# Kernel optimization log

Hardware: AMD Instinct MI355X
Metric: run time of the kernel (lower is better)

Reference implementation:

```python
import jax, jax.numpy as jnp
import numpy as np

M = 0.25
GAMMA = 256.0
HARD_W = 2.0
O_P = 1.0 + M
O_N = -M
DELTA_P = 1.0 - M
DELTA_N = M
NEG_BIG = -1e30  # masked-out fill for logsumexp (finite to keep grads NaN-free)


def setup_inputs() -> dict:
    key = jax.random.key(0)
    k1, k2 = jax.random.split(key)
    inputs = jax.random.normal(k1, (4096, 512), dtype=jnp.float32)
    targets = jax.random.randint(k2, (4096,), 0, 64, dtype=jnp.int64)
    return {"inputs": inputs, "targets": targets}


def reference(inputs, targets):
    n = inputs.shape[0]
    x = inputs / jnp.linalg.norm(inputs, axis=1, keepdims=True)  # L2 normalize
    sim = x @ x.T                                                # [n, n]

    same = targets[:, None] == targets[None, :]
    eye = jnp.eye(n, dtype=bool)
    pos_mask = same & ~eye
    neg_mask = ~same
    npos = pos_mask.sum(axis=1)
    nneg = neg_mask.sum(axis=1)

    sim_d = jax.lax.stop_gradient(sim)  # alphas are detached in the original
    alpha_p = jax.nn.relu(O_P - sim_d)
    alpha_n = jax.nn.relu(sim_d - O_N)

    # hard mining: scale alpha at hardest positive (min sim) / hardest negative (max sim)
    idx = jnp.arange(n)
    hard_p = jnp.argmin(jnp.where(pos_mask, sim_d, jnp.inf), axis=1)
    hard_n = jnp.argmax(jnp.where(neg_mask, sim_d, -jnp.inf), axis=1)
    hit_p = (idx[None, :] == hard_p[:, None]) & (npos > 1)[:, None]
    hit_n = (idx[None, :] == hard_n[:, None]) & (nneg > 1)[:, None]
    alpha_p = alpha_p * jnp.where(hit_p, HARD_W, 1.0)
    alpha_n = alpha_n * jnp.where(hit_n, HARD_W, 1.0)

    pos_term = jnp.where(pos_mask, -GAMMA * alpha_p * (sim - DELTA_P), NEG_BIG)
    neg_term = jnp.where(neg_mask, GAMMA * alpha_n * (sim - DELTA_N), NEG_BIG)
    lse_p = jax.nn.logsumexp(pos_term, axis=1)
    lse_n = jax.nn.logsumexp(neg_term, axis=1)

    valid = (npos > 0) & (nneg > 0)
    per_row = jnp.where(valid, jax.nn.softplus(lse_p + lse_n), 0.0)
    n_valid = jnp.maximum(valid.sum(), 1)
    return per_row.sum() / n_valid.astype(per_row.dtype)
```

## Files before the change

kernel.cpp:

```cpp
#include <hip/hip_runtime.h>


#define GAMMA_ 256.0f
#define OP_ 1.25f
#define ON_ (-0.25f)
#define DP_ 0.75f
#define DN_ 0.25f
#define MASKT_ (-1.0e4f)

constexpr int N_ = 4096;
constexpr int D_ = 512;
constexpr int AST_ = 520;
constexpr int CCH_ = 8;

typedef __bf16 bf16x8 __attribute__((ext_vector_type(8)));
typedef float  f32x4  __attribute__((ext_vector_type(4)));

__device__ __forceinline__ float pos_term(float s) {
    return -GAMMA_ * fmaxf(OP_ - s, 0.0f) * (s - DP_);
}
__device__ __forceinline__ float neg_term(float s) {
    return  GAMMA_ * fmaxf(s - ON_, 0.0f) * (s - DN_);
}
__device__ __forceinline__ void lse_merge(float m2, float S2, float& m, float& S) {
    float mm = fmaxf(m, m2);
    S = S * __expf(m - mm) + S2 * __expf(m2 - mm);
    m = mm;
}
__device__ __forceinline__ unsigned short f2bf(float f) {
    unsigned int u = __float_as_uint(f);
    unsigned int r = u + 0x7FFFu + ((u >> 16) & 1u);
    return (unsigned short)(r >> 16);
}

__global__ __launch_bounds__(256) void k_norm(const float* __restrict__ in,
                                              unsigned short* __restrict__ xb,
                                              float* __restrict__ acc) {
    const int row  = blockIdx.x * 4 + (threadIdx.x >> 6);
    const int lane = threadIdx.x & 63;
    const float4* src = (const float4*)(in + (size_t)row * D_) + lane * 2;
    float4 a = src[0], b = src[1];
    float ss = a.x*a.x + a.y*a.y + a.z*a.z + a.w*a.w
             + b.x*b.x + b.y*b.y + b.z*b.z + b.w*b.w;
    #pragma unroll
    for (int d = 32; d >= 1; d >>= 1) ss += __shfl_xor(ss, d);
    float rn = 1.0f / sqrtf(ss);
    float v[8] = {a.x, a.y, a.z, a.w, b.x, b.y, b.z, b.w};
    union { uint4 u; unsigned short us[8]; } pk;
    #pragma unroll
    for (int k = 0; k < 8; ++k) pk.us[k] = f2bf(v[k] * rn);
    *((uint4*)(xb + (size_t)row * D_) + lane) = pk.u;
    if (blockIdx.x == 0 && threadIdx.x < 2) acc[threadIdx.x] = 0.0f;
}

__global__ __launch_bounds__(256, 3) void k_mainB(const unsigned short* __restrict__ xb,
                                                  const int* __restrict__ tg,
                                                  float* __restrict__ part) {
    constexpr int COLS = N_ / CCH_;
    constexpr int NST  = COLS / 16;
    __shared__ __align__(16) unsigned short Bs[2][16][AST_];

    const int tid  = threadIdx.x;
    const int wave = tid >> 6, lane = tid & 63;
    const int n16  = lane & 15, quad = lane >> 4;
    const int rg   = (int)blockIdx.x >> 3;
    const int cc   = (int)blockIdx.x & 7;
    const int rowBase = rg * 64 + wave * 16;
    const int colBase = cc * COLS;

    bf16x8 af[16];
    {
        const bf16x8* ap = (const bf16x8*)(xb + (size_t)(rowBase + n16) * D_ + quad * 8);
        #pragma unroll
        for (int kk = 0; kk < 16; ++kk) af[kk] = ap[kk * 4];
    }
    int ir[4], tr[4];
    #pragma unroll
    for (int r = 0; r < 4; ++r) { ir[r] = rowBase + quad * 4 + r; tr[r] = tg[ir[r]]; }

    float m_p[4], S_p[4], m_n[4], S_n[4], mnp[4], mxn[4], sc[4];
    #pragma unroll
    for (int r = 0; r < 4; ++r) {
        m_p[r] = 0.f; S_p[r] = 0.f; m_n[r] = 0.f; S_n[r] = 0.f;
        mnp[r] = 2.0f; mxn[r] = -2.0f; sc[r] = 0.f;
    }

    uint4 pf0, pf1, pf2, pf3; int pftc;
    {
        const uint4* g = (const uint4*)(xb + (size_t)colBase * D_);
        pf0 = g[tid]; pf1 = g[256 + tid]; pf2 = g[512 + tid]; pf3 = g[768 + tid];
        pftc = tg[colBase + n16];
    }

    #pragma unroll 1
    for (int s = 0; s < NST; ++s) {
        const int b = s & 1;
        const int j0 = colBase + s * 16;
        {
            int q;
            q = tid;       *(uint4*)&Bs[b][q >> 6][(q & 63) * 8] = pf0;
            q = 256 + tid; *(uint4*)&Bs[b][q >> 6][(q & 63) * 8] = pf1;
            q = 512 + tid; *(uint4*)&Bs[b][q >> 6][(q & 63) * 8] = pf2;
            q = 768 + tid; *(uint4*)&Bs[b][q >> 6][(q & 63) * 8] = pf3;
        }
        const int tc = pftc;
        if (s + 1 < NST) {
            const uint4* g = (const uint4*)(xb + (size_t)(j0 + 16) * D_);
            pf0 = g[tid]; pf1 = g[256 + tid]; pf2 = g[512 + tid]; pf3 = g[768 + tid];
            pftc = tg[j0 + 16 + n16];
        }
        __syncthreads();

        f32x4 a0 = {0.f, 0.f, 0.f, 0.f}, a1 = {0.f, 0.f, 0.f, 0.f};
        #pragma unroll
        for (int kk = 0; kk < 8; ++kk) {
            bf16x8 bf0 = *(const bf16x8*)&Bs[b][n16][(2 * kk) * 32 + quad * 8];
            bf16x8 bf1 = *(const bf16x8*)&Bs[b][n16][(2 * kk + 1) * 32 + quad * 8];
            a0 = __builtin_amdgcn_mfma_f32_16x16x32_bf16(af[2 * kk],     bf0, a0, 0, 0, 0);
            a1 = __builtin_amdgcn_mfma_f32_16x16x32_bf16(af[2 * kk + 1], bf1, a1, 0, 0, 0);
        }

        const int jcol = j0 + n16;
        #pragma unroll
        for (int r = 0; r < 4; ++r) {
            float s_ = a0[r] + a1[r];
            bool samec = (tr[r] == tc);
            bool posm  = samec && (jcol != ir[r]);
            float tp = posm  ? pos_term(s_) : MASKT_;
            float tn = samec ? MASKT_ : neg_term(s_);
            float mm = fmaxf(m_p[r], tp);
            S_p[r] = S_p[r] * __expf(m_p[r] - mm) + __expf(tp - mm); m_p[r] = mm;
            mm = fmaxf(m_n[r], tn);
            S_n[r] = S_n[r] * __expf(m_n[r] - mm) + __expf(tn - mm); m_n[r] = mm;
            sc[r] += samec ? 1.0f : 0.0f;
            mnp[r] = fminf(mnp[r], posm ? s_ : 2.0f);
            mxn[r] = fmaxf(mxn[r], samec ? -2.0f : s_);
        }
    }

    #pragma unroll
    for (int r = 0; r < 4; ++r) {
        #pragma unroll
        for (int d = 1; d <= 8; d <<= 1) {
            lse_merge(__shfl_xor(m_p[r], d), __shfl_xor(S_p[r], d), m_p[r], S_p[r]);
            lse_merge(__shfl_xor(m_n[r], d), __shfl_xor(S_n[r], d), m_n[r], S_n[r]);
            mnp[r] = fminf(mnp[r], __shfl_xor(mnp[r], d));
            mxn[r] = fmaxf(mxn[r], __shfl_xor(mxn[r], d));
            sc[r] += __shfl_xor(sc[r], d);
        }
    }
    if (n16 == 0) {
        #pragma unroll
        for (int r = 0; r < 4; ++r) {
            float4* P = (float4*)part + ((size_t)ir[r] * CCH_ + cc) * 2;
            P[0] = make_float4(m_p[r], S_p[r], m_n[r], S_n[r]);
            P[1] = make_float4(mnp[r], mxn[r], sc[r], 0.0f);
        }
    }
}

__global__ __launch_bounds__(256) void k_reduceB(const float* __restrict__ part,
                                                 float* __restrict__ acc) {
    const int row = blockIdx.x * 256 + threadIdx.x;
    const float4* P = (const float4*)part + (size_t)row * CCH_ * 2;
    float m_p = 0.f, S_p = 0.f, m_n = 0.f, S_n = 0.f;
    float mnp = 2.0f, mxn = -2.0f, sct = 0.f;
    #pragma unroll
    for (int c = 0; c < CCH_; ++c) {
        float4 a = P[2 * c], b = P[2 * c + 1];
        lse_merge(a.x, a.y, m_p, S_p);
        lse_merge(a.z, a.w, m_n, S_n);
        mnp = fminf(mnp, b.x); mxn = fmaxf(mxn, b.y); sct += b.z;
    }
    float loss = 0.f, vld = 0.f;
    float np2 = sct - 1.0f, nn2 = (float)N_ - sct;
    if (np2 > 0.5f && nn2 > 0.5f) {
        if (np2 > 1.5f) {
            float t1 = pos_term(mnp), t2 = 2.0f * t1;
            float mm = fmaxf(m_p, t2);
            S_p = S_p * __expf(m_p - mm) + __expf(t2 - mm) - __expf(t1 - mm);
            m_p = mm;
        }
        if (nn2 > 1.5f) {
            float t1 = neg_term(mxn), t2 = 2.0f * t1;
            float mm = fmaxf(m_n, t2);
            S_n = S_n * __expf(m_n - mm) + __expf(t2 - mm) - __expf(t1 - mm);
            m_n = mm;
        }
        float z = (m_p + __logf(S_p)) + (m_n + __logf(S_n));
        loss = fmaxf(z, 0.0f) + log1pf(__expf(-fabsf(z)));
        vld = 1.0f;
    }
    #pragma unroll
    for (int d = 32; d >= 1; d >>= 1) { loss += __shfl_xor(loss, d); vld += __shfl_xor(vld, d); }
    if ((threadIdx.x & 63) == 0) { atomicAdd(&acc[0], loss); atomicAdd(&acc[1], vld); }
}

__global__ void k_final(const float* __restrict__ acc, float* __restrict__ out) {
    if (threadIdx.x == 0) out[0] = acc[0] / fmaxf(acc[1], 1.0f);
}

__global__ void k_sentinel(float* __restrict__ out) {
    if (threadIdx.x == 0) out[0] = -12345.0f;
}

__global__ __launch_bounds__(1024, 4) void k_main3(const unsigned short* __restrict__ xb,
                                                   const int* __restrict__ tg,
                                                   float* __restrict__ acc_g) {
    __shared__ __align__(16) unsigned short As[16 * AST_];
    __shared__ float sm[16][16][8];
    const int tid  = threadIdx.x;
    const int wave = tid >> 6, lane = tid & 63;
    const int n16  = lane & 15, quad = lane >> 4;
    const int rowBase = blockIdx.x * 16;
    {
        int row = tid >> 6, c = tid & 63;
        *(uint4*)&As[row * AST_ + c * 8] =
            *(const uint4*)(xb + (size_t)(rowBase + row) * D_ + c * 8);
    }
    int ir[4], tr[4];
    #pragma unroll
    for (int r = 0; r < 4; ++r) { ir[r] = rowBase + quad * 4 + r; tr[r] = tg[ir[r]]; }
    float m_p[4], S_p[4], m_n[4], S_n[4], mnp[4], mxn[4], sc[4];
    #pragma unroll
    for (int r = 0; r < 4; ++r) {
        m_p[r] = 0.f; S_p[r] = 0.f; m_n[r] = 0.f; S_n[r] = 0.f;
        mnp[r] = 2.0f; mxn[r] = -2.0f; sc[r] = 0.f;
    }
    __syncthreads();
    const unsigned short* Af = &As[n16 * AST_ + quad * 8];
    #pragma unroll 1
    for (int t = wave; t < N_ / 16; t += 16) {
        const int jcol = t * 16 + n16;
        const int tc = tg[jcol];
        const bf16x8* bp = (const bf16x8*)(xb + (size_t)jcol * D_ + quad * 8);
        bf16x8 bf[16];
        #pragma unroll
        for (int kk = 0; kk < 16; ++kk) bf[kk] = bp[kk * 4];
        f32x4 a0 = {0.f, 0.f, 0.f, 0.f}, a1 = {0.f, 0.f, 0.f, 0.f};
        #pragma unroll
        for (int kk = 0; kk < 8; ++kk) {
            bf16x8 af0 = *(const bf16x8*)(Af + (2 * kk) * 32);
            bf16x8 af1 = *(const bf16x8*)(Af + (2 * kk + 1) * 32);
            a0 = __builtin_amdgcn_mfma_f32_16x16x32_bf16(af0, bf[2 * kk],     a0, 0, 0, 0);
            a1 = __builtin_amdgcn_mfma_f32_16x16x32_bf16(af1, bf[2 * kk + 1], a1, 0, 0, 0);
        }
        #pragma unroll
        for (int r = 0; r < 4; ++r) {
            float s = a0[r] + a1[r];
            bool samec = (tr[r] == tc);
            bool posm  = samec && (jcol != ir[r]);
            float tp = posm  ? pos_term(s) : MASKT_;
            float tn = samec ? MASKT_ : neg_term(s);
            float mm = fmaxf(m_p[r], tp);
            S_p[r] = S_p[r] * __expf(m_p[r] - mm) + __expf(tp - mm); m_p[r] = mm;
            mm = fmaxf(m_n[r], tn);
            S_n[r] = S_n[r] * __expf(m_n[r] - mm) + __expf(tn - mm); m_n[r] = mm;
            sc[r] += samec ? 1.0f : 0.0f;
            mnp[r] = fminf(mnp[r], posm ? s : 2.0f);
            mxn[r] = fmaxf(mxn[r], samec ? -2.0f : s);
        }
    }
    #pragma unroll
    for (int r = 0; r < 4; ++r) {
        #pragma unroll
        for (int d = 1; d <= 8; d <<= 1) {
            lse_merge(__shfl_xor(m_p[r], d), __shfl_xor(S_p[r], d), m_p[r], S_p[r]);
            lse_merge(__shfl_xor(m_n[r], d), __shfl_xor(S_n[r], d), m_n[r], S_n[r]);
            mnp[r] = fminf(mnp[r], __shfl_xor(mnp[r], d));
            mxn[r] = fmaxf(mxn[r], __shfl_xor(mxn[r], d));
            sc[r] += __shfl_xor(sc[r], d);
        }
    }
    if (n16 == 0) {
        #pragma unroll
        for (int r = 0; r < 4; ++r) {
            float* q = sm[wave][quad * 4 + r];
            q[0] = m_p[r]; q[1] = S_p[r]; q[2] = m_n[r]; q[3] = S_n[r];
            q[4] = mnp[r]; q[5] = mxn[r]; q[6] = sc[r];
        }
    }
    __syncthreads();
    if (tid < 64) {
        const int L = tid & 15;
        float m_p2 = 0.f, S_p2 = 0.f, m_n2 = 0.f, S_n2 = 0.f;
        float mnp2 = 2.0f, mxn2 = -2.0f, sct = 0.f;
        #pragma unroll
        for (int w = 0; w < 16; ++w) {
            const float* q = sm[w][L];
            lse_merge(q[0], q[1], m_p2, S_p2);
            lse_merge(q[2], q[3], m_n2, S_n2);
            mnp2 = fminf(mnp2, q[4]); mxn2 = fmaxf(mxn2, q[5]);
            sct += q[6];
        }
        float loss = 0.f, vld = 0.f;
        float np2 = sct - 1.0f, nn2 = (float)N_ - sct;
        if (tid < 16 && np2 > 0.5f && nn2 > 0.5f) {
            if (np2 > 1.5f) {
                float t1 = pos_term(mnp2), t2 = 2.0f * t1;
                float mm = fmaxf(m_p2, t2);
                S_p2 = S_p2 * __expf(m_p2 - mm) + __expf(t2 - mm) - __expf(t1 - mm);
                m_p2 = mm;
            }
            if (nn2 > 1.5f) {
                float t1 = neg_term(mxn2), t2 = 2.0f * t1;
                float mm = fmaxf(m_n2, t2);
                S_n2 = S_n2 * __expf(m_n2 - mm) + __expf(t2 - mm) - __expf(t1 - mm);
                m_n2 = mm;
            }
            float z = (m_p2 + __logf(S_p2)) + (m_n2 + __logf(S_n2));
            loss = fmaxf(z, 0.0f) + log1pf(__expf(-fabsf(z)));
            vld = 1.0f;
        }
        #pragma unroll
        for (int d = 32; d >= 1; d >>= 1) {
            loss += __shfl_xor(loss, d); vld += __shfl_xor(vld, d);
        }
        if (tid == 0) { atomicAdd(&acc_g[0], loss); atomicAdd(&acc_g[1], vld); }
    }
}

extern "C" void kernel_launch(void* const* d_in, const int* in_sizes, int n_in,
                              void* d_out, int out_size, void* d_ws, size_t ws_size,
                              hipStream_t stream) {
    const float* in = (const float*)d_in[0];
    const int*   tg = (const int*)d_in[1];
    constexpr size_t MB = 1024 * 1024;
    unsigned short* xb = (unsigned short*)d_ws;

    if (ws_size >= 5 * MB + 64) {
        float* part = (float*)((char*)d_ws + 4 * MB);
        float* acc  = (float*)((char*)d_ws + 5 * MB);
        hipLaunchKernelGGL(k_norm,    dim3(N_ / 4),   dim3(256), 0, stream, in, xb, acc);
        hipLaunchKernelGGL(k_mainB,   dim3(64 * CCH_), dim3(256), 0, stream, xb, tg, part);
        hipLaunchKernelGGL(k_reduceB, dim3(N_ / 256), dim3(256), 0, stream, part, acc);
        hipLaunchKernelGGL(k_final,   dim3(1),        dim3(64),  0, stream, acc, (float*)d_out);
    } else if (ws_size >= 4 * MB + 64) {
        float* acc = (float*)((char*)d_ws + 4 * MB);
        hipLaunchKernelGGL(k_norm,  dim3(N_ / 4),  dim3(256),  0, stream, in, xb, acc);
        hipLaunchKernelGGL(k_main3, dim3(N_ / 16), dim3(1024), 0, stream, xb, tg, acc);
        hipLaunchKernelGGL(k_final, dim3(1),       dim3(64),   0, stream, acc, (float*)d_out);
    } else {
        hipLaunchKernelGGL(k_sentinel, dim3(1), dim3(64), 0, stream, (float*)d_out);
    }
}
```

Baseline: 113.6 us.

## Simplify circle-loss terms algebraically, swizzle LDS, and split columns into 16 chunks

The pos/neg logits are rewritten as quadratics with the constant offset removed (256(s-1)^2 and 256 s^2, shifted by -16), and the online logsumexp now uses a branch so only one exp is computed per element. Same-class counts are no longer accumulated in the main loop; the reduce kernel builds a label histogram in shared memory instead. The column chunk count goes from 8 to 16, occupancy is raised to 4 blocks per CU, LDS uses an XOR-swizzled flat layout to avoid bank conflicts, and the loop is unrolled by two with a static double buffer. Each partial record shrinks to one float4 by storing the min/max similarity in place of the running max, which the reduce step recomputes. In exchange the reduce does more work per row, and the branchy update may diverge within a wave.

```diff
diff --git a/kernel.cpp b/kernel.cpp
--- a/kernel.cpp
+++ b/kernel.cpp
@@ -2,25 +2,23 @@
 
 
 #define GAMMA_ 256.0f
-#define OP_ 1.25f
-#define ON_ (-0.25f)
-#define DP_ 0.75f
-#define DN_ 0.25f
 #define MASKT_ (-1.0e4f)
 
 constexpr int N_ = 4096;
 constexpr int D_ = 512;
 constexpr int AST_ = 520;
-constexpr int CCH_ = 8;
+constexpr int CCH_ = 16;
 
 typedef __bf16 bf16x8 __attribute__((ext_vector_type(8)));
 typedef float  f32x4  __attribute__((ext_vector_type(4)));
 
-__device__ __forceinline__ float pos_term(float s) {
-    return -GAMMA_ * fmaxf(OP_ - s, 0.0f) * (s - DP_);
-}
-__device__ __forceinline__ float neg_term(float s) {
-    return  GAMMA_ * fmaxf(s - ON_, 0.0f) * (s - DN_);
+__device__ __forceinline__ float pos_q(float s) {
+    float d = s - 1.0f;
+    return fmaf(d * d, 256.0f, -16.0f);
+}
+__device__ __forceinline__ float neg_q(float s) {
+    float q = fmaf(s * s, 256.0f, -16.0f);
+    return (s >= -0.25f) ? q : 0.0f;
 }
 __device__ __forceinline__ void lse_merge(float m2, float S2, float& m, float& S) {
     float mm = fmaxf(m, m2);
@@ -53,20 +51,19 @@
     if (blockIdx.x == 0 && threadIdx.x < 2) acc[threadIdx.x] = 0.0f;
 }
 
-__global__ __launch_bounds__(256, 3) void k_mainB(const unsigned short* __restrict__ xb,
+__global__ __launch_bounds__(256, 4) void k_mainC(const unsigned short* __restrict__ xb,
                                                   const int* __restrict__ tg,
                                                   float* __restrict__ part) {
-    constexpr int COLS = N_ / CCH_;
-    constexpr int NST  = COLS / 16;
-    __shared__ __align__(16) unsigned short Bs[2][16][AST_];
+    constexpr int NST = 16;
+    __shared__ uint4 Bs[2][1024];
 
     const int tid  = threadIdx.x;
     const int wave = tid >> 6, lane = tid & 63;
     const int n16  = lane & 15, quad = lane >> 4;
-    const int rg   = (int)blockIdx.x >> 3;
-    const int cc   = (int)blockIdx.x & 7;
+    const int rg   = (int)blockIdx.x >> 4;
+    const int cc   = (int)blockIdx.x & 15;
     const int rowBase = rg * 64 + wave * 16;
-    const int colBase = cc * COLS;
+    const int colBase = cc * 256;
 
     bf16x8 af[16];
     {
@@ -78,64 +75,76 @@
     #pragma unroll
     for (int r = 0; r < 4; ++r) { ir[r] = rowBase + quad * 4 + r; tr[r] = tg[ir[r]]; }
 
-    float m_p[4], S_p[4], m_n[4], S_n[4], mnp[4], mxn[4], sc[4];
+    int wa[4];
+    #pragma unroll
+    for (int p = 0; p < 4; ++p) {
+        int kkw = lane >> 2;
+        int f   = (lane & 3) * 16 + (wave + 4 * p);
+        wa[p]   = kkw * 64 + (f ^ (kkw & 7));
+    }
+    int rva[8];
+    #pragma unroll
+    for (int c = 0; c < 8; ++c) rva[c] = lane ^ c;
+
+    float m_p[4], S_p[4], m_n[4], S_n[4], mnp[4], mxn[4];
     #pragma unroll
     for (int r = 0; r < 4; ++r) {
         m_p[r] = 0.f; S_p[r] = 0.f; m_n[r] = 0.f; S_n[r] = 0.f;
-        mnp[r] = 2.0f; mxn[r] = -2.0f; sc[r] = 0.f;
-    }
-
-    uint4 pf0, pf1, pf2, pf3; int pftc;
-    {
-        const uint4* g = (const uint4*)(xb + (size_t)colBase * D_);
-        pf0 = g[tid]; pf1 = g[256 + tid]; pf2 = g[512 + tid]; pf3 = g[768 + tid];
-        pftc = tg[colBase + n16];
-    }
-
-    #pragma unroll 1
-    for (int s = 0; s < NST; ++s) {
-        const int b = s & 1;
-        const int j0 = colBase + s * 16;
-        {
-            int q;
-            q = tid;       *(uint4*)&Bs[b][q >> 6][(q & 63) * 8] = pf0;
-            q = 256 + tid; *(uint4*)&Bs[b][q >> 6][(q & 63) * 8] = pf1;
-            q = 512 + tid; *(uint4*)&Bs[b][q >> 6][(q & 63) * 8] = pf2;
-            q = 768 + tid; *(uint4*)&Bs[b][q >> 6][(q & 63) * 8] = pf3;
-        }
-        const int tc = pftc;
-        if (s + 1 < NST) {
-            const uint4* g = (const uint4*)(xb + (size_t)(j0 + 16) * D_);
-            pf0 = g[tid]; pf1 = g[256 + tid]; pf2 = g[512 + tid]; pf3 = g[768 + tid];
-            pftc = tg[j0 + 16 + n16];
+        mnp[r] = 2.0f; mxn[r] = -2.0f;
+    }
+
+    const uint4* gsrc = (const uint4*)(xb + (size_t)colBase * D_);
+    uint4 pf0 = gsrc[tid], pf1 = gsrc[256 + tid], pf2 = gsrc[512 + tid], pf3 = gsrc[768 + tid];
+    int tc_cur = tg[colBase + n16], tc_nxt = 0;
+
+    auto do_stage = [&](int s, int b, bool pre) {
+        uint4* Bp = &Bs[b][0];
+        Bp[wa[0]] = pf0; Bp[wa[1]] = pf1; Bp[wa[2]] = pf2; Bp[wa[3]] = pf3;
+        if (pre) {
+            const uint4* g2 = gsrc + (s + 1) * 1024;
+            pf0 = g2[tid]; pf1 = g2[256 + tid]; pf2 = g2[512 + tid]; pf3 = g2[768 + tid];
+            tc_nxt = tg[colBase + (s + 1) * 16 + n16];
         }
         __syncthreads();
 
         f32x4 a0 = {0.f, 0.f, 0.f, 0.f}, a1 = {0.f, 0.f, 0.f, 0.f};
         #pragma unroll
         for (int kk = 0; kk < 8; ++kk) {
-            bf16x8 bf0 = *(const bf16x8*)&Bs[b][n16][(2 * kk) * 32 + quad * 8];
-            bf16x8 bf1 = *(const bf16x8*)&Bs[b][n16][(2 * kk + 1) * 32 + quad * 8];
+            bf16x8 bf0 = *(const bf16x8*)&Bp[(2 * kk) * 64 + rva[(2 * kk) & 7]];
+            bf16x8 bf1 = *(const bf16x8*)&Bp[(2 * kk + 1) * 64 + rva[(2 * kk + 1) & 7]];
             a0 = __builtin_amdgcn_mfma_f32_16x16x32_bf16(af[2 * kk],     bf0, a0, 0, 0, 0);
             a1 = __builtin_amdgcn_mfma_f32_16x16x32_bf16(af[2 * kk + 1], bf1, a1, 0, 0, 0);
         }
 
-        const int jcol = j0 + n16;
+        const int jcol = colBase + s * 16 + n16;
+        const int tcv = tc_cur;
         #pragma unroll
         for (int r = 0; r < 4; ++r) {
             float s_ = a0[r] + a1[r];
-            bool samec = (tr[r] == tc);
+            bool samec = (tr[r] == tcv);
             bool posm  = samec && (jcol != ir[r]);
-            float tp = posm  ? pos_term(s_) : MASKT_;
-            float tn = samec ? MASKT_ : neg_term(s_);
-            float mm = fmaxf(m_p[r], tp);
-            S_p[r] = S_p[r] * __expf(m_p[r] - mm) + __expf(tp - mm); m_p[r] = mm;
-            mm = fmaxf(m_n[r], tn);
-            S_n[r] = S_n[r] * __expf(m_n[r] - mm) + __expf(tn - mm); m_n[r] = mm;
-            sc[r] += samec ? 1.0f : 0.0f;
+            float tp = posm ? pos_q(s_) : MASKT_;
+            if (tp > m_p[r]) {
+                S_p[r] = fmaf(S_p[r], __expf(m_p[r] - tp), 1.0f); m_p[r] = tp;
+            } else {
+                S_p[r] += __expf(tp - m_p[r]);
+            }
             mnp[r] = fminf(mnp[r], posm ? s_ : 2.0f);
+            float tn = samec ? MASKT_ : neg_q(s_);
+            if (tn > m_n[r]) {
+                S_n[r] = fmaf(S_n[r], __expf(m_n[r] - tn), 1.0f); m_n[r] = tn;
+            } else {
+                S_n[r] += __expf(tn - m_n[r]);
+            }
             mxn[r] = fmaxf(mxn[r], samec ? -2.0f : s_);
         }
+        tc_cur = tc_nxt;
+    };
+
+    #pragma unroll 1
+    for (int it = 0; it < NST / 2; ++it) {
+        do_stage(2 * it,     0, true);
+        do_stage(2 * it + 1, 1, it < NST / 2 - 1);
     }
 
     #pragma unroll
@@ -146,54 +155,62 @@
             lse_merge(__shfl_xor(m_n[r], d), __shfl_xor(S_n[r], d), m_n[r], S_n[r]);
             mnp[r] = fminf(mnp[r], __shfl_xor(mnp[r], d));
             mxn[r] = fmaxf(mxn[r], __shfl_xor(mxn[r], d));
-            sc[r] += __shfl_xor(sc[r], d);
         }
     }
     if (n16 == 0) {
         #pragma unroll
         for (int r = 0; r < 4; ++r) {
-            float4* P = (float4*)part + ((size_t)ir[r] * CCH_ + cc) * 2;
-            P[0] = make_float4(m_p[r], S_p[r], m_n[r], S_n[r]);
-            P[1] = make_float4(mnp[r], mxn[r], sc[r], 0.0f);
-        }
-    }
-}
-
-__global__ __launch_bounds__(256) void k_reduceB(const float* __restrict__ part,
+            ((float4*)part)[(size_t)ir[r] * CCH_ + cc] =
+                make_float4(mnp[r], S_p[r], mxn[r], S_n[r]);
+        }
+    }
+}
+
+__global__ __launch_bounds__(256) void k_reduceC(const float* __restrict__ part,
+                                                 const int* __restrict__ tg,
                                                  float* __restrict__ acc) {
-    const int row = blockIdx.x * 256 + threadIdx.x;
-    const float4* P = (const float4*)part + (size_t)row * CCH_ * 2;
-    float m_p = 0.f, S_p = 0.f, m_n = 0.f, S_n = 0.f;
-    float mnp = 2.0f, mxn = -2.0f, sct = 0.f;
+    __shared__ int hist[64];
+    const int tid = threadIdx.x;
+    if (tid < 64) hist[tid] = 0;
+    __syncthreads();
+    for (int i = tid; i < N_; i += 256) atomicAdd(&hist[tg[i]], 1);
+    __syncthreads();
+
+    const int row = blockIdx.x * 256 + tid;
+    const float4* P = (const float4*)part + (size_t)row * CCH_;
+    float M_p = 0.f, Sp = 0.f, M_n = 0.f, Sn = 0.f, mnp = 2.0f, mxn = -2.0f;
     #pragma unroll
     for (int c = 0; c < CCH_; ++c) {
-        float4 a = P[2 * c], b = P[2 * c + 1];
-        lse_merge(a.x, a.y, m_p, S_p);
-        lse_merge(a.z, a.w, m_n, S_n);
-        mnp = fminf(mnp, b.x); mxn = fmaxf(mxn, b.y); sct += b.z;
-    }
+        float4 a = P[c];
+        float mc = (a.x < 1.5f) ? fmaxf(pos_q(a.x), 0.0f) : 0.0f;
+        lse_merge(mc, a.y, M_p, Sp);
+        float mn = (a.z > -1.5f) ? fmaxf(neg_q(a.z), 0.0f) : 0.0f;
+        lse_merge(mn, a.w, M_n, Sn);
+        mnp = fminf(mnp, a.x); mxn = fmaxf(mxn, a.z);
+    }
+    const int cnt = hist[tg[row]];
+    float np2 = (float)(cnt - 1), nn2 = (float)(N_ - cnt);
     float loss = 0.f, vld = 0.f;
-    float np2 = sct - 1.0f, nn2 = (float)N_ - sct;
     if (np2 > 0.5f && nn2 > 0.5f) {
         if (np2 > 1.5f) {
-            float t1 = pos_term(mnp), t2 = 2.0f * t1;
-            float mm = fmaxf(m_p, t2);
-            S_p = S_p * __expf(m_p - mm) + __expf(t2 - mm) - __expf(t1 - mm);
-            m_p = mm;
+            float t1 = pos_q(mnp), t2 = 2.0f * t1;
+            float mm = fmaxf(M_p, t2);
+            Sp = Sp * __expf(M_p - mm) + __expf(t2 - mm) - __expf(t1 - mm);
+            M_p = mm;
         }
         if (nn2 > 1.5f) {
-            float t1 = neg_term(mxn), t2 = 2.0f * t1;
-            float mm = fmaxf(m_n, t2);
-            S_n = S_n * __expf(m_n - mm) + __expf(t2 - mm) - __expf(t1 - mm);
-            m_n = mm;
-        }
-        float z = (m_p + __logf(S_p)) + (m_n + __logf(S_n));
+            float t1 = neg_q(mxn), t2 = 2.0f * t1;
+            float mm = fmaxf(M_n, t2);
+            Sn = Sn * __expf(M_n - mm) + __expf(t2 - mm) - __expf(t1 - mm);
+            M_n = mm;
+        }
+        float z = (M_p + __logf(Sp)) + (M_n + __logf(Sn));
         loss = fmaxf(z, 0.0f) + log1pf(__expf(-fabsf(z)));
         vld = 1.0f;
     }
     #pragma unroll
     for (int d = 32; d >= 1; d >>= 1) { loss += __shfl_xor(loss, d); vld += __shfl_xor(vld, d); }
-    if ((threadIdx.x & 63) == 0) { atomicAdd(&acc[0], loss); atomicAdd(&acc[1], vld); }
+    if ((tid & 63) == 0) { atomicAdd(&acc[0], loss); atomicAdd(&acc[1], vld); }
 }
 
 __global__ void k_final(const float* __restrict__ acc, float* __restrict__ out) {
@@ -250,8 +267,8 @@
             float s = a0[r] + a1[r];
             bool samec = (tr[r] == tc);
             bool posm  = samec && (jcol != ir[r]);
-            float tp = posm  ? pos_term(s) : MASKT_;
-            float tn = samec ? MASKT_ : neg_term(s);
+            float tp = posm  ? pos_q(s) : MASKT_;
+            float tn = samec ? MASKT_ : neg_q(s);
             float mm = fmaxf(m_p[r], tp);
             S_p[r] = S_p[r] * __expf(m_p[r] - mm) + __expf(tp - mm); m_p[r] = mm;
             mm = fmaxf(m_n[r], tn);
@@ -297,13 +314,13 @@
         float np2 = sct - 1.0f, nn2 = (float)N_ - sct;
         if (tid < 16 && np2 > 0.5f && nn2 > 0.5f) {
             if (np2 > 1.5f) {
-                float t1 = pos_term(mnp2), t2 = 2.0f * t1;
+                float t1 = pos_q(mnp2), t2 = 2.0f * t1;
                 float mm = fmaxf(m_p2, t2);
                 S_p2 = S_p2 * __expf(m_p2 - mm) + __expf(t2 - mm) - __expf(t1 - mm);
                 m_p2 = mm;
             }
             if (nn2 > 1.5f) {
-                float t1 = neg_term(mxn2), t2 = 2.0f * t1;
+                float t1 = neg_q(mxn2), t2 = 2.0f * t1;
                 float mm = fmaxf(m_n2, t2);
                 S_n2 = S_n2 * __expf(m_n2 - mm) + __expf(t2 - mm) - __expf(t1 - mm);
                 m_n2 = mm;
@@ -331,10 +348,10 @@
     if (ws_size >= 5 * MB + 64) {
         float* part = (float*)((char*)d_ws + 4 * MB);
         float* acc  = (float*)((char*)d_ws + 5 * MB);
-        hipLaunchKernelGGL(k_norm,    dim3(N_ / 4),   dim3(256), 0, stream, in, xb, acc);
-        hipLaunchKernelGGL(k_mainB,   dim3(64 * CCH_), dim3(256), 0, stream, xb, tg, part);
-        hipLaunchKernelGGL(k_reduceB, dim3(N_ / 256), dim3(256), 0, stream, part, acc);
-        hipLaunchKernelGGL(k_final,   dim3(1),        dim3(64),  0, stream, acc, (float*)d_out);
+        hipLaunchKernelGGL(k_norm,    dim3(N_ / 4),    dim3(256), 0, stream, in, xb, acc);
+        hipLaunchKernelGGL(k_mainC,   dim3(64 * CCH_), dim3(256), 0, stream, xb, tg, part);
+        hipLaunchKernelGGL(k_reduceC, dim3(N_ / 256),  dim3(256), 0, stream, part, tg, acc);
+        hipLaunchKernelGGL(k_final,   dim3(1),         dim3(64),  0, stream, acc, (float*)d_out);
     } else if (ws_size >= 4 * MB + 64) {
         float* acc = (float*)((char*)d_ws + 4 * MB);
         hipLaunchKernelGGL(k_norm,  dim3(N_ / 4),  dim3(256),  0, stream, in, xb, acc);
```

Measured after the change: 160.2 us. 41.1% more time.
